# Kernel tuning notes

Hardware: AMD Instinct MI355X
Metric: run time of the kernel (lower is better)

The kernel has to match this reference:

```python
import jax, jax.numpy as jnp
import numpy as np

N, E, IN = 50000, 800000, 64
HC, FC1, FC2, FC3, OUT = 96, 256, 128, 64, 8
EPS = 1e-5


def setup_inputs() -> dict:
    key = jax.random.key(0)
    ks = jax.random.split(key, 24)
    def lin(k, fi, fo):
        # kaiming_uniform with relu gain: bound = sqrt(6/fi)
        b = np.sqrt(6.0 / fi)
        return jax.random.uniform(k, (fi, fo), jnp.float32, -b, b)
    inp = {
        'x': jax.random.normal(ks[0], (N, IN), jnp.float32),
        'edge_index': jax.random.randint(ks[1], (2, E), 0, N, jnp.int64),
        'w1': lin(ks[2], IN, HC), 'b1': jnp.zeros((HC,), jnp.float32),
        'g1': jax.random.uniform(ks[3], (HC,), jnp.float32, 0.5, 1.5), 'be1': jax.random.normal(ks[4], (HC,), jnp.float32) * 0.1,
        'w2': lin(ks[5], HC, HC), 'b2': jnp.zeros((HC,), jnp.float32),
        'g2': jax.random.uniform(ks[6], (HC,), jnp.float32, 0.5, 1.5), 'be2': jax.random.normal(ks[7], (HC,), jnp.float32) * 0.1,
        'w3': lin(ks[8], HC, HC), 'b3': jnp.zeros((HC,), jnp.float32),
        'g3': jax.random.uniform(ks[9], (HC,), jnp.float32, 0.5, 1.5), 'be3': jax.random.normal(ks[10], (HC,), jnp.float32) * 0.1,
        'lw1': lin(ks[11], HC, FC1), 'lb1': jnp.zeros((FC1,), jnp.float32),
        'lw2': lin(ks[12], FC1, FC2), 'lb2': jnp.zeros((FC2,), jnp.float32),
        'lw3': lin(ks[13], FC2, FC3), 'lb3': jnp.zeros((FC3,), jnp.float32),
        'lw4': lin(ks[14], FC3, OUT), 'lb4': jnp.zeros((OUT,), jnp.float32),
    }
    return inp


def _gcn(x, w, b, src, dst, norm):
    # GCNConv: out[dst] += norm_e * (x @ w)[src]; then + bias
    h = x @ w
    msg = h[src] * norm[:, None]
    return jax.ops.segment_sum(msg, dst, num_segments=N) + b


def _bn_eval(x, g, be):
    # eval-mode BatchNorm1d with running_mean=0, running_var=1
    return x / jnp.sqrt(1.0 + EPS) * g + be


def reference(x, edge_index, w1, b1, g1, be1, w2, b2, g2, be2, w3, b3, g3, be3,
              lw1, lb1, lw2, lb2, lw3, lb3, lw4, lb4):
    loops = jnp.arange(N, dtype=edge_index.dtype)
    src = jnp.concatenate([edge_index[0], loops])
    dst = jnp.concatenate([edge_index[1], loops])
    deg = jax.ops.segment_sum(jnp.ones_like(src, jnp.float32), dst, num_segments=N)
    dinv = jax.lax.rsqrt(deg)  # deg >= 1 due to self loops
    norm = dinv[src] * dinv[dst]

    h = jax.nn.relu(_bn_eval(_gcn(x, w1, b1, src, dst, norm), g1, be1))
    h = jax.nn.relu(_bn_eval(_gcn(h, w2, b2, src, dst, norm), g2, be2))
    h = jax.nn.relu(_bn_eval(_gcn(h, w3, b3, src, dst, norm), g3, be3))
    h = jax.nn.relu(h @ lw1 + lb1)
    h = jax.nn.relu(h @ lw2 + lb2)
    h = jax.nn.relu(h @ lw3 + lb3)
    return h @ lw4 + lb4
```

## Files before the change

### kernel.cpp

```cpp
#include <hip/hip_runtime.h>


#define GN 50000
#define GE 800000
#define NPART 98
#define PSLOT 9216
#define CHK 2048

typedef __attribute__((ext_vector_type(8))) short bf16x8;
typedef __attribute__((ext_vector_type(4))) float floatx4;

__device__ __forceinline__ float ar1_b2f(unsigned short h) {
    return __uint_as_float(((unsigned)h) << 16);
}
__device__ __forceinline__ unsigned short ar1_f2b(float f) {
    unsigned u = __float_as_uint(f);
    u = u + 0x7FFFu + ((u >> 16) & 1u);
    return (unsigned short)(u >> 16);
}

__global__ void ar1_detect(const int* ei, const unsigned short* xw,
                           int* flagI, int* flagF, int* gcur) {
    __shared__ int cnt;
    if (threadIdx.x == 0) cnt = 0;
    __syncthreads();
    if (blockIdx.x == 0) {
        if ((int)threadIdx.x < NPART) gcur[threadIdx.x] = 0;
        if (ei[2 * threadIdx.x + 1] != 0) atomicAdd(&cnt, 1);
        __syncthreads();
        if (threadIdx.x == 0) flagI[0] = (cnt < 8) ? 1 : 0;
    } else {
        unsigned short w = xw[2 * threadIdx.x];
        int ex = (w >> 7) & 0xFF;
        if (w == 0 || (ex >= 90 && ex <= 150)) atomicAdd(&cnt, 1);
        __syncthreads();
        if (threadIdx.x == 0) flagF[0] = (cnt > 200) ? 0 : 1;
    }
}

__global__ __launch_bounds__(256)
void ar1_part(const int* __restrict__ ei, const int* __restrict__ flagI,
              int* __restrict__ gcur, unsigned int* __restrict__ pairs, int E) {
    __shared__ int cnt[NPART], base[NPART], cur[NPART];
    int tid = (int)threadIdx.x;
    for (int i = tid; i < NPART; i += 256) { cnt[i] = 0; cur[i] = 0; }
    __syncthreads();
    int is64 = flagI[0];
    int e0 = (int)blockIdx.x * CHK;
    unsigned pk[8]; int q[8];
#pragma unroll
    for (int k = 0; k < 8; k++) {
        int e = e0 + k * 256 + tid;
        q[k] = -1; pk[k] = 0;
        if (e < E) {
            int s = is64 ? ei[2 * e] : ei[e];
            int d = is64 ? ei[2 * (E + e)] : ei[E + e];
            if ((unsigned)s < (unsigned)GN && (unsigned)d < (unsigned)GN) {
                int qq = d >> 9;
                q[k] = qq;
                pk[k] = (unsigned)s | ((unsigned)(d & 511) << 17);
                atomicAdd(&cnt[qq], 1);
            }
        }
    }
    __syncthreads();
    for (int i = tid; i < NPART; i += 256)
        base[i] = (cnt[i] > 0) ? atomicAdd(&gcur[i], cnt[i]) : 0;
    __syncthreads();
#pragma unroll
    for (int k = 0; k < 8; k++) {
        if (q[k] >= 0) {
            int r = base[q[k]] + atomicAdd(&cur[q[k]], 1);
            if (r < PSLOT) pairs[(size_t)q[k] * PSLOT + r] = pk[k];
        }
    }
}

__global__ void ar1_pscan(const int* gcur, int* pbase) {
    __shared__ int sm[128];
    int tid = (int)threadIdx.x;
    int v = (tid < NPART) ? gcur[tid] : 0;
    sm[tid] = v;
    __syncthreads();
    for (int off = 1; off < 128; off <<= 1) {
        int t = (tid >= off) ? sm[tid - off] : 0;
        __syncthreads();
        sm[tid] += t;
        __syncthreads();
    }
    if (tid < NPART) pbase[tid] = sm[tid] - v;
}

__global__ __launch_bounds__(256)
void ar1_csr(const unsigned int* __restrict__ pairs, const int* __restrict__ gcur,
             const int* __restrict__ pbase, int* __restrict__ csr,
             int* __restrict__ indeg, int* __restrict__ offs,
             float* __restrict__ dinv) {
    __shared__ int ncnt[512], pre[512], cur[512], psum[16];
    int p = (int)blockIdx.x, tid = (int)threadIdx.x;
    int cntE = gcur[p];
    if (cntE > PSLOT) cntE = PSLOT;
    int gbase = pbase[p];
    for (int i = tid; i < 512; i += 256) ncnt[i] = 0;
    __syncthreads();
    const unsigned int* pp = pairs + (size_t)p * PSLOT;
    for (int i = tid; i < cntE; i += 256) atomicAdd(&ncnt[pp[i] >> 17], 1);
    __syncthreads();
    if (tid < 16) {
        int s = 0;
        for (int j = tid * 32; j < tid * 32 + 32; j++) { pre[j] = s; s += ncnt[j]; }
        psum[tid] = s;
    }
    __syncthreads();
    if (tid == 0) {
        int s = 0;
        for (int j = 0; j < 16; j++) { int t = psum[j]; psum[j] = s; s += t; }
    }
    __syncthreads();
    if (tid < 16)
        for (int j = tid * 32; j < tid * 32 + 32; j++) pre[j] += psum[tid];
    __syncthreads();
    for (int j = tid; j < 512; j += 256) {
        cur[j] = pre[j];
        int node = p * 512 + j;
        if (node < GN) {
            indeg[node] = ncnt[j];
            offs[node] = gbase + pre[j];
            dinv[node] = rsqrtf((float)(ncnt[j] + 1));
        }
    }
    __syncthreads();
    for (int i = tid; i < cntE; i += 256) {
        unsigned v = pp[i];
        int r = atomicAdd(&cur[v >> 17], 1);
        csr[gbase + r] = (int)(v & 0x1FFFFu);
    }
}

struct PackAll {
    const void* src[7];
    unsigned short* dst[7];
    int K[7], M[7], start[8];
};
struct SmallCvt {
    const void* src[4];
    float* dst[4];
    int n[4];
    const void* gb[9];
    float* ss[6];
};

__global__ void Arthur1_16458314678864_kernel(PackAll pa, SmallCvt sc,
                                              const int* flagF) {
    int b = (int)blockIdx.x;
    int f = flagF[0];
    if (b < 45) {
        int frag_g = b * 4 + ((int)threadIdx.x >> 6);
        if (frag_g >= 178) return;
        int w = 0;
        while (w < 6 && frag_g >= pa.start[w + 1]) w++;
        int frag = frag_g - pa.start[w];
        int K = pa.K[w], M = pa.M[w];
        int lane = (int)threadIdx.x & 63;
        int nch = K >> 5;
        int t = frag / nch, c = frag - t * nch;
        int n = t * 16 + (lane & 15);
        int k0 = c * 32 + (lane >> 4) * 8;
        unsigned short* o = pa.dst[w] + ((size_t)frag * 64 + lane) * 8;
        for (int j = 0; j < 8; j++) {
            unsigned short v = 0;
            if (n < M) {
                int idx = (k0 + j) * M + n;
                v = f ? ar1_f2b(((const float*)pa.src[w])[idx])
                      : ((const unsigned short*)pa.src[w])[idx];
            }
            o[j] = v;
        }
    } else {
        const float C = 0.9999950000374997f;
        for (int s = 0; s < 4; s++) {
            for (int i = threadIdx.x; i < sc.n[s]; i += 256) {
                float v = f ? ((const float*)sc.src[s])[i]
                            : ar1_b2f(((const unsigned short*)sc.src[s])[i]);
                sc.dst[s][i] = v;
            }
        }
        for (int k = 0; k < 3; k++) {
            for (int i = threadIdx.x; i < 96; i += 256) {
                float bb, g, be;
                if (f) {
                    bb = ((const float*)sc.gb[3 * k + 0])[i];
                    g  = ((const float*)sc.gb[3 * k + 1])[i];
                    be = ((const float*)sc.gb[3 * k + 2])[i];
                } else {
                    bb = ar1_b2f(((const unsigned short*)sc.gb[3 * k + 0])[i]);
                    g  = ar1_b2f(((const unsigned short*)sc.gb[3 * k + 1])[i]);
                    be = ar1_b2f(((const unsigned short*)sc.gb[3 * k + 2])[i]);
                }
                sc.ss[2 * k + 0][i] = C * g;
                sc.ss[2 * k + 1][i] = bb * C * g + be;
            }
        }
    }
}

template <int NT>
__global__ __launch_bounds__(256, 2)
void ar1_mfma(const unsigned short* __restrict__ A,
              const unsigned short* __restrict__ Bp,
              const float* __restrict__ scale, const float* __restrict__ shift,
              unsigned short* __restrict__ C, int K, int Astride, int Cstride) {
    int tid = (int)threadIdx.x;
    int wv = tid >> 6, lane = tid & 63;
    int mb = ((int)blockIdx.x * 4 + wv) * 16;
    int m = lane & 15, quad = lane >> 4;
    int arow = mb + m;
    if (arow >= GN) arow = GN - 1;
    const unsigned short* Aptr = A + (size_t)arow * Astride + quad * 8;
    int nch = K >> 5;

    floatx4 acc[NT];
#pragma unroll
    for (int t = 0; t < NT; t++) acc[t] = (floatx4){0.f, 0.f, 0.f, 0.f};

    for (int c = 0; c < nch; c++) {
        bf16x8 a = *((const bf16x8*)(Aptr + c * 32));
#pragma unroll
        for (int t = 0; t < NT; t++) {
            bf16x8 b = *((const bf16x8*)(Bp + ((size_t)(t * nch + c) * 64 + lane) * 8));
            acc[t] = __builtin_amdgcn_mfma_f32_16x16x32_bf16(a, b, acc[t], 0, 0, 0);
        }
    }

#pragma unroll
    for (int t = 0; t < NT; t++) {
#pragma unroll
        for (int r = 0; r < 4; r++) {
            int row = mb + quad * 4 + r;
            int col = t * 16 + m;
            if (row < GN) {
                float v = acc[t][r] * scale[col] + shift[col];
                C[(size_t)row * Cstride + col] = ar1_f2b(fmaxf(v, 0.f));
            }
        }
    }
}

__global__ __launch_bounds__(256, 2)
void ar1_mlp(const unsigned short* __restrict__ A,
             const unsigned short* __restrict__ b3,
             const unsigned short* __restrict__ b4,
             const unsigned short* __restrict__ b5,
             const unsigned short* __restrict__ b6,
             const float* __restrict__ lb0, const float* __restrict__ lb1,
             const float* __restrict__ lb2, const float* __restrict__ lb3,
             void* __restrict__ out, const int* __restrict__ f32out) {
    __shared__ unsigned short H1[64 * 264];
    __shared__ unsigned short H2[64 * 136];
    __shared__ unsigned short H3[64 * 72];
    int tid = (int)threadIdx.x, wv = tid >> 6, lane = tid & 63;
    int m = lane & 15, quad = lane >> 4;
    int mb = (int)blockIdx.x * 64 + wv * 16;
    int lwv = wv * 16;

    {
        int arow = mb + m; if (arow >= GN) arow = GN - 1;
        const unsigned short* Ap = A + (size_t)arow * 96 + quad * 8;
        floatx4 acc[16];
#pragma unroll
        for (int t = 0; t < 16; t++) acc[t] = (floatx4){0.f, 0.f, 0.f, 0.f};
        for (int c = 0; c < 3; c++) {
            bf16x8 a = *((const bf16x8*)(Ap + c * 32));
#pragma unroll
            for (int t = 0; t < 16; t++) {
                bf16x8 b = *((const bf16x8*)(b3 + ((size_t)(t * 3 + c) * 64 + lane) * 8));
                acc[t] = __builtin_amdgcn_mfma_f32_16x16x32_bf16(a, b, acc[t], 0, 0, 0);
            }
        }
#pragma unroll
        for (int t = 0; t < 16; t++)
#pragma unroll
            for (int r = 0; r < 4; r++) {
                int lr = lwv + quad * 4 + r, col = t * 16 + m;
                H1[lr * 264 + col] = ar1_f2b(fmaxf(acc[t][r] + lb0[col], 0.f));
            }
    }
    {
        const unsigned short* Hp = H1 + (size_t)(lwv + m) * 264 + quad * 8;
        floatx4 acc[8];
#pragma unroll
        for (int t = 0; t < 8; t++) acc[t] = (floatx4){0.f, 0.f, 0.f, 0.f};
        for (int c = 0; c < 8; c++) {
            bf16x8 a = *((const bf16x8*)(Hp + c * 32));
#pragma unroll
            for (int t = 0; t < 8; t++) {
                bf16x8 b = *((const bf16x8*)(b4 + ((size_t)(t * 8 + c) * 64 + lane) * 8));
                acc[t] = __builtin_amdgcn_mfma_f32_16x16x32_bf16(a, b, acc[t], 0, 0, 0);
            }
        }
#pragma unroll
        for (int t = 0; t < 8; t++)
#pragma unroll
            for (int r = 0; r < 4; r++) {
                int lr = lwv + quad * 4 + r, col = t * 16 + m;
                H2[lr * 136 + col] = ar1_f2b(fmaxf(acc[t][r] + lb1[col], 0.f));
            }
    }
    {
        const unsigned short* Hp = H2 + (size_t)(lwv + m) * 136 + quad * 8;
        floatx4 acc[4];
#pragma unroll
        for (int t = 0; t < 4; t++) acc[t] = (floatx4){0.f, 0.f, 0.f, 0.f};
        for (int c = 0; c < 4; c++) {
            bf16x8 a = *((const bf16x8*)(Hp + c * 32));
#pragma unroll
            for (int t = 0; t < 4; t++) {
                bf16x8 b = *((const bf16x8*)(b5 + ((size_t)(t * 4 + c) * 64 + lane) * 8));
                acc[t] = __builtin_amdgcn_mfma_f32_16x16x32_bf16(a, b, acc[t], 0, 0, 0);
            }
        }
#pragma unroll
        for (int t = 0; t < 4; t++)
#pragma unroll
            for (int r = 0; r < 4; r++) {
                int lr = lwv + quad * 4 + r, col = t * 16 + m;
                H3[lr * 72 + col] = ar1_f2b(fmaxf(acc[t][r] + lb2[col], 0.f));
            }
    }
    {
        const unsigned short* Hp = H3 + (size_t)(lwv + m) * 72 + quad * 8;
        floatx4 acc = (floatx4){0.f, 0.f, 0.f, 0.f};
        for (int c = 0; c < 2; c++) {
            bf16x8 a = *((const bf16x8*)(Hp + c * 32));
            bf16x8 b = *((const bf16x8*)(b6 + ((size_t)c * 64 + lane) * 8));
            acc = __builtin_amdgcn_mfma_f32_16x16x32_bf16(a, b, acc, 0, 0, 0);
        }
        int wf32 = f32out[0];
#pragma unroll
        for (int r = 0; r < 4; r++) {
            int row = mb + quad * 4 + r;
            if (row < GN && m < 8) {
                float v = acc[r] + lb3[m];
                if (wf32) ((float*)out)[(size_t)row * 8 + m] = v;
                else ((unsigned short*)out)[(size_t)row * 8 + m] = ar1_f2b(v);
            }
        }
    }
}

__global__ __launch_bounds__(256, 8)
void ar1_agg64(const void* __restrict__ Xv, const int* __restrict__ offs,
               const int* __restrict__ indeg, const int* __restrict__ csr,
               const float* __restrict__ dinv, const int* __restrict__ flagF,
               unsigned short* __restrict__ Out) {
    int wv = (int)threadIdx.x >> 6, lane = (int)threadIdx.x & 63;
    int node = (int)blockIdx.x * 4 + wv;
    if (node >= GN) return;
    int chunk = lane & 7;
    int eslot = lane >> 3;
    float di = dinv[node];
    int off = offs[node], cnt = indeg[node];
    int f = flagF[0];
    const unsigned short* X16 = (const unsigned short*)Xv;
    const float* X32 = (const float*)Xv;

    float acc[8];
#pragma unroll
    for (int j = 0; j < 8; j++) acc[j] = 0.f;

    for (int base = 0; base < cnt; base += 16) {
        int ss[2]; float ww[2];
#pragma unroll
        for (int k = 0; k < 2; k++) {
            int e = base + k * 8 + eslot;
            int s = node; float w = 0.f;
            if (e < cnt) {
                s = csr[off + e];
                if ((unsigned)s >= (unsigned)GN) s = node;
                w = dinv[s] * di;
            }
            ss[k] = s; ww[k] = w;
        }
#pragma unroll
        for (int k = 0; k < 2; k++) {
            float hv[8];
            if (f) {
                floatx4 a = *((const floatx4*)(X32 + (size_t)ss[k] * 64 + chunk * 8));
                floatx4 b = *((const floatx4*)(X32 + (size_t)ss[k] * 64 + chunk * 8 + 4));
#pragma unroll
                for (int j = 0; j < 4; j++) { hv[j] = a[j]; hv[4 + j] = b[j]; }
            } else {
                bf16x8 h = *((const bf16x8*)(X16 + (size_t)ss[k] * 64 + chunk * 8));
#pragma unroll
                for (int j = 0; j < 8; j++) hv[j] = ar1_b2f((unsigned short)h[j]);
            }
#pragma unroll
            for (int j = 0; j < 8; j++) acc[j] += ww[k] * hv[j];
        }
    }

#pragma unroll
    for (int j = 0; j < 8; j++) {
        acc[j] += __shfl_xor(acc[j], 8, 64);
        acc[j] += __shfl_xor(acc[j], 16, 64);
        acc[j] += __shfl_xor(acc[j], 32, 64);
    }

    if (eslot == 0) {
        float hv[8];
        if (f) {
            floatx4 a = *((const floatx4*)(X32 + (size_t)node * 64 + chunk * 8));
            floatx4 b = *((const floatx4*)(X32 + (size_t)node * 64 + chunk * 8 + 4));
#pragma unroll
            for (int j = 0; j < 4; j++) { hv[j] = a[j]; hv[4 + j] = b[j]; }
        } else {
            bf16x8 h = *((const bf16x8*)(X16 + (size_t)node * 64 + chunk * 8));
#pragma unroll
            for (int j = 0; j < 8; j++) hv[j] = ar1_b2f((unsigned short)h[j]);
        }
#pragma unroll
        for (int j = 0; j < 8; j++) {
            float v = acc[j] + di * di * hv[j];
            Out[(size_t)node * 64 + chunk * 8 + j] = ar1_f2b(v);
        }
    }
}

__global__ __launch_bounds__(256, 8)
void ar1_agg96(const unsigned short* __restrict__ H, const int* __restrict__ offs,
               const int* __restrict__ indeg, const int* __restrict__ csr,
               const float* __restrict__ dinv, unsigned short* __restrict__ Out) {
    int wv = (int)threadIdx.x >> 6, lane = (int)threadIdx.x & 63;
    int node = (int)blockIdx.x * 4 + wv;
    if (node >= GN) return;
    int chunk = lane % 12;
    int eslot = lane / 12;
    int active = (lane < 48) ? 1 : 0;
    float di = dinv[node];
    int off = offs[node], cnt = indeg[node];

    float acc[8];
#pragma unroll
    for (int j = 0; j < 8; j++) acc[j] = 0.f;

    if (active) {
        for (int base = 0; base < cnt; base += 16) {
            int ss[4]; float ww[4]; bf16x8 hh[4];
#pragma unroll
            for (int k = 0; k < 4; k++) {
                int e = base + k * 4 + eslot;
                int s = node; float w = 0.f;
                if (e < cnt) {
                    s = csr[off + e];
                    if ((unsigned)s >= (unsigned)GN) s = node;
                    w = dinv[s] * di;
                }
                ss[k] = s; ww[k] = w;
            }
#pragma unroll
            for (int k = 0; k < 4; k++)
                hh[k] = *((const bf16x8*)(H + (size_t)ss[k] * 96 + chunk * 8));
#pragma unroll
            for (int k = 0; k < 4; k++)
#pragma unroll
                for (int j = 0; j < 8; j++)
                    acc[j] += ww[k] * ar1_b2f((unsigned short)hh[k][j]);
        }
    }

#pragma unroll
    for (int j = 0; j < 8; j++) {
        float a1 = __shfl(acc[j], lane + 12, 64);
        float a2 = __shfl(acc[j], lane + 24, 64);
        float a3 = __shfl(acc[j], lane + 36, 64);
        acc[j] += a1 + a2 + a3;
    }

    if (lane < 12) {
        bf16x8 hs = *((const bf16x8*)(H + (size_t)node * 96 + chunk * 8));
#pragma unroll
        for (int j = 0; j < 8; j++) {
            float v = acc[j] + di * di * ar1_b2f((unsigned short)hs[j]);
            Out[(size_t)node * 96 + chunk * 8 + j] = ar1_f2b(v);
        }
    }
}

extern "C" void kernel_launch(void* const* d_in, const int* in_sizes, int n_in,
                              void* d_out, int out_size, void* d_ws, size_t ws_size,
                              hipStream_t stream) {
    (void)in_sizes; (void)n_in; (void)out_size;

    char* p = (char*)d_ws;
    unsigned short* bufA = (unsigned short*)p; p += (size_t)GN * 96 * 2;
    unsigned short* bufC = (unsigned short*)p; p += (size_t)GN * 96 * 2;
    unsigned int* pairs = (unsigned int*)p; p += (size_t)NPART * PSLOT * 4;
    int* indeg  = (int*)p;    p += (size_t)GN * 4;
    int* offs   = (int*)p;    p += (size_t)GN * 4;
    float* dinv = (float*)p;  p += (size_t)GN * 4;
    int* csr    = (int*)p;    p += (size_t)GE * 4;
    int* gcur   = (int*)p;    p += 1024;
    int* pbase  = (int*)p;    p += 1024;
    int* flagI  = (int*)p;    p += 1024;
    int* flagF  = (int*)p;    p += 1024;
    unsigned short* bpArena = (unsigned short*)p; p += 91136 * 2;
    float* fArena = (float*)p; p += 2048 * 4;
    size_t need = (size_t)(p - (char*)d_ws);
    if (ws_size < need) {
        hipMemsetAsync(d_out, 0x41, (size_t)GN * 8 * 2, stream);
        return;
    }

    unsigned short* bp[7];
    int bpn[7] = {6144, 9216, 9216, 24576, 32768, 8192, 1024};
    {
        unsigned short* q = bpArena;
        for (int i = 0; i < 7; i++) { bp[i] = q; q += bpn[i]; }
    }

    float* lb[4]; float* ss[6];
    {
        float* q = fArena;
        int ln[4] = {256, 128, 64, 8};
        for (int i = 0; i < 4; i++) { lb[i] = q; q += ln[i]; }
        for (int i = 0; i < 6; i++) { ss[i] = q; q += 96; }
    }

    const int* ei = (const int*)d_in[1];

    ar1_detect<<<2, 256, 0, stream>>>(ei, (const unsigned short*)d_in[0], flagI, flagF, gcur);
    ar1_part<<<(GE + CHK - 1) / CHK, 256, 0, stream>>>(ei, flagI, gcur, pairs, GE);
    ar1_pscan<<<1, 128, 0, stream>>>(gcur, pbase);
    ar1_csr<<<NPART, 256, 0, stream>>>(pairs, gcur, pbase, csr, indeg, offs, dinv);

    {
        PackAll pa;
        int wsrc[7] = {2, 6, 10, 14, 16, 18, 20};
        int Ks[7] = {64, 96, 96, 96, 256, 128, 64};
        int Ms[7] = {96, 96, 96, 256, 128, 64, 8};
        int cum = 0;
        for (int i = 0; i < 7; i++) {
            pa.src[i] = d_in[wsrc[i]]; pa.dst[i] = bp[i];
            pa.K[i] = Ks[i]; pa.M[i] = Ms[i];
            pa.start[i] = cum;
            cum += (Ms[i] + 15) / 16 * (Ks[i] / 32);
        }
        pa.start[7] = cum;
        SmallCvt sc;
        int lsrc[4] = {15, 17, 19, 21};
        int ln[4] = {256, 128, 64, 8};
        for (int i = 0; i < 4; i++) { sc.src[i] = d_in[lsrc[i]]; sc.dst[i] = lb[i]; sc.n[i] = ln[i]; }
        int gsrc[9] = {3, 4, 5, 7, 8, 9, 11, 12, 13};
        for (int i = 0; i < 9; i++) sc.gb[i] = d_in[gsrc[i]];
        for (int i = 0; i < 6; i++) sc.ss[i] = ss[i];
        Arthur1_16458314678864_kernel<<<46, 256, 0, stream>>>(pa, sc, flagF);
    }

    const int GB = (GN + 63) / 64;
    const int AB = GN / 4;

    ar1_agg64<<<AB, 256, 0, stream>>>(d_in[0], offs, indeg, csr, dinv, flagF, bufC);
    ar1_mfma<6><<<GB, 256, 0, stream>>>(bufC, bp[0], ss[0], ss[1], bufA, 64, 64, 96);
    ar1_agg96<<<AB, 256, 0, stream>>>(bufA, offs, indeg, csr, dinv, bufC);
    ar1_mfma<6><<<GB, 256, 0, stream>>>(bufC, bp[1], ss[2], ss[3], bufA, 96, 96, 96);
    ar1_agg96<<<AB, 256, 0, stream>>>(bufA, offs, indeg, csr, dinv, bufC);
    ar1_mfma<6><<<GB, 256, 0, stream>>>(bufC, bp[2], ss[4], ss[5], bufA, 96, 96, 96);

    ar1_mlp<<<GB, 256, 0, stream>>>(bufA, bp[3], bp[4], bp[5], bp[6],
                                    lb[0], lb[1], lb[2], lb[3], d_out, flagF);
}
```

Baseline: 324.7 us.

## Fuse neighbor aggregation with MFMA linear transform per 64-node tile

Each aggregation kernel now processes 64 nodes per block (16 per wave, sequentially), stores the aggregated bf16 rows in LDS, then runs the MFMA weight multiply with BN/ReLU epilogue from LDS. This removes three separate GEMM launches and the global round-trip of the aggregated intermediate. In exchange, each block holds 16x fewer waves in flight per node, so there is less parallelism to hide gather latency, and the loop over 16 nodes per wave is serialized. No barrier is needed because each wave reads only its own 16 rows.

```diff
diff --git a/kernel.cpp b/kernel.cpp
--- a/kernel.cpp
+++ b/kernel.cpp
@@ -204,43 +204,204 @@
     }
 }
 
-template <int NT>
-__global__ __launch_bounds__(256, 2)
-void ar1_mfma(const unsigned short* __restrict__ A,
+__global__ __launch_bounds__(256, 8)
+void ar1_ag64(const void* __restrict__ Xv, const int* __restrict__ offs,
+              const int* __restrict__ indeg, const int* __restrict__ csr,
+              const float* __restrict__ dinv, const int* __restrict__ flagF,
               const unsigned short* __restrict__ Bp,
               const float* __restrict__ scale, const float* __restrict__ shift,
-              unsigned short* __restrict__ C, int K, int Astride, int Cstride) {
-    int tid = (int)threadIdx.x;
-    int wv = tid >> 6, lane = tid & 63;
-    int mb = ((int)blockIdx.x * 4 + wv) * 16;
+              unsigned short* __restrict__ C) {
+    __shared__ unsigned short AL[64 * 72];
+    int tid = (int)threadIdx.x, wv = tid >> 6, lane = tid & 63;
+    int nb = (int)blockIdx.x * 64;
+    int f = flagF[0];
+    const unsigned short* X16 = (const unsigned short*)Xv;
+    const float* X32 = (const float*)Xv;
+    int chunk = lane & 7;
+    int eslot = lane >> 3;
+
+    for (int t = 0; t < 16; t++) {
+        int node = nb + wv * 16 + t;
+        if (node >= GN) break;
+        float di = dinv[node];
+        int off = offs[node], cnt = indeg[node];
+        float acc[8];
+#pragma unroll
+        for (int j = 0; j < 8; j++) acc[j] = 0.f;
+
+        for (int base = 0; base < cnt; base += 16) {
+            int ss[2]; float ww[2];
+#pragma unroll
+            for (int k = 0; k < 2; k++) {
+                int e = base + k * 8 + eslot;
+                int s = node; float w = 0.f;
+                if (e < cnt) {
+                    s = csr[off + e];
+                    if ((unsigned)s >= (unsigned)GN) s = node;
+                    w = dinv[s] * di;
+                }
+                ss[k] = s; ww[k] = w;
+            }
+#pragma unroll
+            for (int k = 0; k < 2; k++) {
+                float hv[8];
+                if (f) {
+                    floatx4 a = *((const floatx4*)(X32 + (size_t)ss[k] * 64 + chunk * 8));
+                    floatx4 b = *((const floatx4*)(X32 + (size_t)ss[k] * 64 + chunk * 8 + 4));
+#pragma unroll
+                    for (int j = 0; j < 4; j++) { hv[j] = a[j]; hv[4 + j] = b[j]; }
+                } else {
+                    bf16x8 h = *((const bf16x8*)(X16 + (size_t)ss[k] * 64 + chunk * 8));
+#pragma unroll
+                    for (int j = 0; j < 8; j++) hv[j] = ar1_b2f((unsigned short)h[j]);
+                }
+#pragma unroll
+                for (int j = 0; j < 8; j++) acc[j] += ww[k] * hv[j];
+            }
+        }
+
+#pragma unroll
+        for (int j = 0; j < 8; j++) {
+            acc[j] += __shfl_xor(acc[j], 8, 64);
+            acc[j] += __shfl_xor(acc[j], 16, 64);
+            acc[j] += __shfl_xor(acc[j], 32, 64);
+        }
+
+        if (eslot == 0) {
+            float hv[8];
+            if (f) {
+                floatx4 a = *((const floatx4*)(X32 + (size_t)node * 64 + chunk * 8));
+                floatx4 b = *((const floatx4*)(X32 + (size_t)node * 64 + chunk * 8 + 4));
+#pragma unroll
+                for (int j = 0; j < 4; j++) { hv[j] = a[j]; hv[4 + j] = b[j]; }
+            } else {
+                bf16x8 h = *((const bf16x8*)(X16 + (size_t)node * 64 + chunk * 8));
+#pragma unroll
+                for (int j = 0; j < 8; j++) hv[j] = ar1_b2f((unsigned short)h[j]);
+            }
+            bf16x8 o;
+#pragma unroll
+            for (int j = 0; j < 8; j++)
+                o[j] = (short)ar1_f2b(acc[j] + di * di * hv[j]);
+            *((bf16x8*)(AL + (size_t)(wv * 16 + t) * 72 + chunk * 8)) = o;
+        }
+    }
+
     int m = lane & 15, quad = lane >> 4;
-    int arow = mb + m;
-    if (arow >= GN) arow = GN - 1;
-    const unsigned short* Aptr = A + (size_t)arow * Astride + quad * 8;
-    int nch = K >> 5;
-
-    floatx4 acc[NT];
-#pragma unroll
-    for (int t = 0; t < NT; t++) acc[t] = (floatx4){0.f, 0.f, 0.f, 0.f};
-
-    for (int c = 0; c < nch; c++) {
-        bf16x8 a = *((const bf16x8*)(Aptr + c * 32));
-#pragma unroll
-        for (int t = 0; t < NT; t++) {
-            bf16x8 b = *((const bf16x8*)(Bp + ((size_t)(t * nch + c) * 64 + lane) * 8));
+    floatx4 acc[6];
+#pragma unroll
+    for (int t = 0; t < 6; t++) acc[t] = (floatx4){0.f, 0.f, 0.f, 0.f};
+#pragma unroll
+    for (int c = 0; c < 2; c++) {
+        bf16x8 a = *((const bf16x8*)(AL + (size_t)(wv * 16 + m) * 72 + c * 32 + quad * 8));
+#pragma unroll
+        for (int t = 0; t < 6; t++) {
+            bf16x8 b = *((const bf16x8*)(Bp + ((size_t)(t * 2 + c) * 64 + lane) * 8));
             acc[t] = __builtin_amdgcn_mfma_f32_16x16x32_bf16(a, b, acc[t], 0, 0, 0);
         }
     }
-
-#pragma unroll
-    for (int t = 0; t < NT; t++) {
+#pragma unroll
+    for (int t = 0; t < 6; t++) {
 #pragma unroll
         for (int r = 0; r < 4; r++) {
-            int row = mb + quad * 4 + r;
+            int row = nb + wv * 16 + quad * 4 + r;
             int col = t * 16 + m;
             if (row < GN) {
                 float v = acc[t][r] * scale[col] + shift[col];
-                C[(size_t)row * Cstride + col] = ar1_f2b(fmaxf(v, 0.f));
+                C[(size_t)row * 96 + col] = ar1_f2b(fmaxf(v, 0.f));
+            }
+        }
+    }
+}
+
+__global__ __launch_bounds__(256, 8)
+void ar1_ag96(const unsigned short* __restrict__ H, const int* __restrict__ offs,
+              const int* __restrict__ indeg, const int* __restrict__ csr,
+              const float* __restrict__ dinv,
+              const unsigned short* __restrict__ Bp,
+              const float* __restrict__ scale, const float* __restrict__ shift,
+              unsigned short* __restrict__ C) {
+    __shared__ unsigned short AL[64 * 104];
+    int tid = (int)threadIdx.x, wv = tid >> 6, lane = tid & 63;
+    int nb = (int)blockIdx.x * 64;
+    int chunk = lane % 12;
+    int eslot = lane / 12;
+    int active = (lane < 48) ? 1 : 0;
+
+    for (int t = 0; t < 16; t++) {
+        int node = nb + wv * 16 + t;
+        if (node >= GN) break;
+        float di = dinv[node];
+        int off = offs[node], cnt = indeg[node];
+        float acc[8];
+#pragma unroll
+        for (int j = 0; j < 8; j++) acc[j] = 0.f;
+
+        if (active) {
+            for (int base = 0; base < cnt; base += 16) {
+                int ss[4]; float ww[4]; bf16x8 hh[4];
+#pragma unroll
+                for (int k = 0; k < 4; k++) {
+                    int e = base + k * 4 + eslot;
+                    int s = node; float w = 0.f;
+                    if (e < cnt) {
+                        s = csr[off + e];
+                        if ((unsigned)s >= (unsigned)GN) s = node;
+                        w = dinv[s] * di;
+                    }
+                    ss[k] = s; ww[k] = w;
+                }
+#pragma unroll
+                for (int k = 0; k < 4; k++)
+                    hh[k] = *((const bf16x8*)(H + (size_t)ss[k] * 96 + chunk * 8));
+#pragma unroll
+                for (int k = 0; k < 4; k++)
+#pragma unroll
+                    for (int j = 0; j < 8; j++)
+                        acc[j] += ww[k] * ar1_b2f((unsigned short)hh[k][j]);
+            }
+        }
+
+#pragma unroll
+        for (int j = 0; j < 8; j++) {
+            float a1 = __shfl(acc[j], lane + 12, 64);
+            float a2 = __shfl(acc[j], lane + 24, 64);
+            float a3 = __shfl(acc[j], lane + 36, 64);
+            acc[j] += a1 + a2 + a3;
+        }
+
+        if (lane < 12) {
+            bf16x8 hs = *((const bf16x8*)(H + (size_t)node * 96 + chunk * 8));
+            bf16x8 o;
+#pragma unroll
+            for (int j = 0; j < 8; j++)
+                o[j] = (short)ar1_f2b(acc[j] + di * di * ar1_b2f((unsigned short)hs[j]));
+            *((bf16x8*)(AL + (size_t)(wv * 16 + t) * 104 + chunk * 8)) = o;
+        }
+    }
+
+    int m = lane & 15, quad = lane >> 4;
+    floatx4 acc[6];
+#pragma unroll
+    for (int t = 0; t < 6; t++) acc[t] = (floatx4){0.f, 0.f, 0.f, 0.f};
+#pragma unroll
+    for (int c = 0; c < 3; c++) {
+        bf16x8 a = *((const bf16x8*)(AL + (size_t)(wv * 16 + m) * 104 + c * 32 + quad * 8));
+#pragma unroll
+        for (int t = 0; t < 6; t++) {
+            bf16x8 b = *((const bf16x8*)(Bp + ((size_t)(t * 3 + c) * 64 + lane) * 8));
+            acc[t] = __builtin_amdgcn_mfma_f32_16x16x32_bf16(a, b, acc[t], 0, 0, 0);
+        }
+    }
+#pragma unroll
+    for (int t = 0; t < 6; t++) {
+#pragma unroll
+        for (int r = 0; r < 4; r++) {
+            int row = nb + wv * 16 + quad * 4 + r;
+            int col = t * 16 + m;
+            if (row < GN) {
+                float v = acc[t][r] * scale[col] + shift[col];
+                C[(size_t)row * 96 + col] = ar1_f2b(fmaxf(v, 0.f));
             }
         }
     }
@@ -344,144 +505,6 @@
                 if (wf32) ((float*)out)[(size_t)row * 8 + m] = v;
                 else ((unsigned short*)out)[(size_t)row * 8 + m] = ar1_f2b(v);
             }
-        }
-    }
-}
-
-__global__ __launch_bounds__(256, 8)
-void ar1_agg64(const void* __restrict__ Xv, const int* __restrict__ offs,
-               const int* __restrict__ indeg, const int* __restrict__ csr,
-               const float* __restrict__ dinv, const int* __restrict__ flagF,
-               unsigned short* __restrict__ Out) {
-    int wv = (int)threadIdx.x >> 6, lane = (int)threadIdx.x & 63;
-    int node = (int)blockIdx.x * 4 + wv;
-    if (node >= GN) return;
-    int chunk = lane & 7;
-    int eslot = lane >> 3;
-    float di = dinv[node];
-    int off = offs[node], cnt = indeg[node];
-    int f = flagF[0];
-    const unsigned short* X16 = (const unsigned short*)Xv;
-    const float* X32 = (const float*)Xv;
-
-    float acc[8];
-#pragma unroll
-    for (int j = 0; j < 8; j++) acc[j] = 0.f;
-
-    for (int base = 0; base < cnt; base += 16) {
-        int ss[2]; float ww[2];
-#pragma unroll
-        for (int k = 0; k < 2; k++) {
-            int e = base + k * 8 + eslot;
-            int s = node; float w = 0.f;
-            if (e < cnt) {
-                s = csr[off + e];
-                if ((unsigned)s >= (unsigned)GN) s = node;
-                w = dinv[s] * di;
-            }
-            ss[k] = s; ww[k] = w;
-        }
-#pragma unroll
-        for (int k = 0; k < 2; k++) {
-            float hv[8];
-            if (f) {
-                floatx4 a = *((const floatx4*)(X32 + (size_t)ss[k] * 64 + chunk * 8));
-                floatx4 b = *((const floatx4*)(X32 + (size_t)ss[k] * 64 + chunk * 8 + 4));
-#pragma unroll
-                for (int j = 0; j < 4; j++) { hv[j] = a[j]; hv[4 + j] = b[j]; }
-            } else {
-                bf16x8 h = *((const bf16x8*)(X16 + (size_t)ss[k] * 64 + chunk * 8));
-#pragma unroll
-                for (int j = 0; j < 8; j++) hv[j] = ar1_b2f((unsigned short)h[j]);
-            }
-#pragma unroll
-            for (int j = 0; j < 8; j++) acc[j] += ww[k] * hv[j];
-        }
-    }
-
-#pragma unroll
-    for (int j = 0; j < 8; j++) {
-        acc[j] += __shfl_xor(acc[j], 8, 64);
-        acc[j] += __shfl_xor(acc[j], 16, 64);
-        acc[j] += __shfl_xor(acc[j], 32, 64);
-    }
-
-    if (eslot == 0) {
-        float hv[8];
-        if (f) {
-            floatx4 a = *((const floatx4*)(X32 + (size_t)node * 64 + chunk * 8));
-            floatx4 b = *((const floatx4*)(X32 + (size_t)node * 64 + chunk * 8 + 4));
-#pragma unroll
-            for (int j = 0; j < 4; j++) { hv[j] = a[j]; hv[4 + j] = b[j]; }
-        } else {
-            bf16x8 h = *((const bf16x8*)(X16 + (size_t)node * 64 + chunk * 8));
-#pragma unroll
-            for (int j = 0; j < 8; j++) hv[j] = ar1_b2f((unsigned short)h[j]);
-        }
-#pragma unroll
-        for (int j = 0; j < 8; j++) {
-            float v = acc[j] + di * di * hv[j];
-            Out[(size_t)node * 64 + chunk * 8 + j] = ar1_f2b(v);
-        }
-    }
-}
-
-__global__ __launch_bounds__(256, 8)
-void ar1_agg96(const unsigned short* __restrict__ H, const int* __restrict__ offs,
-               const int* __restrict__ indeg, const int* __restrict__ csr,
-               const float* __restrict__ dinv, unsigned short* __restrict__ Out) {
-    int wv = (int)threadIdx.x >> 6, lane = (int)threadIdx.x & 63;
-    int node = (int)blockIdx.x * 4 + wv;
-    if (node >= GN) return;
-    int chunk = lane % 12;
-    int eslot = lane / 12;
-    int active = (lane < 48) ? 1 : 0;
-    float di = dinv[node];
-    int off = offs[node], cnt = indeg[node];
-
-    float acc[8];
-#pragma unroll
-    for (int j = 0; j < 8; j++) acc[j] = 0.f;
-
-    if (active) {
-        for (int base = 0; base < cnt; base += 16) {
-            int ss[4]; float ww[4]; bf16x8 hh[4];
-#pragma unroll
-            for (int k = 0; k < 4; k++) {
-                int e = base + k * 4 + eslot;
-                int s = node; float w = 0.f;
-                if (e < cnt) {
-                    s = csr[off + e];
-                    if ((unsigned)s >= (unsigned)GN) s = node;
-                    w = dinv[s] * di;
-                }
-                ss[k] = s; ww[k] = w;
-            }
-#pragma unroll
-            for (int k = 0; k < 4; k++)
-                hh[k] = *((const bf16x8*)(H + (size_t)ss[k] * 96 + chunk * 8));
-#pragma unroll
-            for (int k = 0; k < 4; k++)
-#pragma unroll
-                for (int j = 0; j < 8; j++)
-                    acc[j] += ww[k] * ar1_b2f((unsigned short)hh[k][j]);
-        }
-    }
-
-#pragma unroll
-    for (int j = 0; j < 8; j++) {
-        float a1 = __shfl(acc[j], lane + 12, 64);
-        float a2 = __shfl(acc[j], lane + 24, 64);
-        float a3 = __shfl(acc[j], lane + 36, 64);
-        acc[j] += a1 + a2 + a3;
-    }
-
-    if (lane < 12) {
-        bf16x8 hs = *((const bf16x8*)(H + (size_t)node * 96 + chunk * 8));
-#pragma unroll
-        for (int j = 0; j < 8; j++) {
-            float v = acc[j] + di * di * ar1_b2f((unsigned short)hs[j]);
-            Out[(size_t)node * 96 + chunk * 8 + j] = ar1_f2b(v);
         }
     }
 }
@@ -556,16 +579,15 @@
         Arthur1_16458314678864_kernel<<<46, 256, 0, stream>>>(pa, sc, flagF);
     }
 
-    const int GB = (GN + 63) / 64;
-    const int AB = GN / 4;
-
-    ar1_agg64<<<AB, 256, 0, stream>>>(d_in[0], offs, indeg, csr, dinv, flagF, bufC);
-    ar1_mfma<6><<<GB, 256, 0, stream>>>(bufC, bp[0], ss[0], ss[1], bufA, 64, 64, 96);
-    ar1_agg96<<<AB, 256, 0, stream>>>(bufA, offs, indeg, csr, dinv, bufC);
-    ar1_mfma<6><<<GB, 256, 0, stream>>>(bufC, bp[1], ss[2], ss[3], bufA, 96, 96, 96);
-    ar1_agg96<<<AB, 256, 0, stream>>>(bufA, offs, indeg, csr, dinv, bufC);
-    ar1_mfma<6><<<GB, 256, 0, stream>>>(bufC, bp[2], ss[4], ss[5], bufA, 96, 96, 96);
-
-    ar1_mlp<<<GB, 256, 0, stream>>>(bufA, bp[3], bp[4], bp[5], bp[6],
+    const int FB = (GN + 63) / 64;
+
+    ar1_ag64<<<FB, 256, 0, stream>>>(d_in[0], offs, indeg, csr, dinv, flagF,
+                                     bp[0], ss[0], ss[1], bufA);
+    ar1_ag96<<<FB, 256, 0, stream>>>(bufA, offs, indeg, csr, dinv,
+                                     bp[1], ss[2], ss[3], bufC);
+    ar1_ag96<<<FB, 256, 0, stream>>>(bufC, offs, indeg, csr, dinv,
+                                     bp[2], ss[4], ss[5], bufA);
+
+    ar1_mlp<<<FB, 256, 0, stream>>>(bufA, bp[3], bp[4], bp[5], bp[6],
                                     lb[0], lb[1], lb[2], lb[3], d_out, flagF);
 }
```

After: 415.4 us. 1.28x slower.
